# Performance work log

Measured on AMD Instinct MI355X. Metric: run time of the kernel, lower is better.

## Reference

```python
import jax, jax.numpy as jnp
import numpy as np

NUM_GRAPHS = 256
N_NODES = 128          # nodes per graph (equal-size graphs)
DEG = 16               # average degree
NUM_EDGES = NUM_GRAPHS * N_NODES * DEG
NUM_HEADS = 8
SCALE = 10.0
INF_REPLACE = 1.0


def setup_inputs() -> dict:
    key = jax.random.key(0)
    k1, k2, k3 = jax.random.split(key, 3)
    # each graph owns a contiguous block of N_NODES global node ids
    eg = jnp.repeat(jnp.arange(NUM_GRAPHS, dtype=jnp.int32), N_NODES * DEG)
    src_loc = jax.random.randint(k1, (NUM_EDGES,), 0, N_NODES, dtype=jnp.int32)
    dst_loc = jax.random.randint(k2, (NUM_EDGES,), 0, N_NODES, dtype=jnp.int32)
    edge_index = jnp.stack([eg * N_NODES + src_loc, eg * N_NODES + dst_loc])  # [2, E]
    edge_weight = jax.random.uniform(k3, (NUM_EDGES,), minval=0.1, maxval=1.0)
    batch = jnp.repeat(jnp.arange(NUM_GRAPHS, dtype=jnp.int32), N_NODES)  # [N_total]
    return {
        'edge_index': edge_index,
        'edge_weight': edge_weight,
        'batch': batch,
        'num_graphs': NUM_GRAPHS,
        'max_num_nodes': N_NODES,
    }


def _shortest_path_bias(edge_index, edge_weight, batch, num_graphs, max_num_nodes):
    G, n = num_graphs, max_num_nodes
    inf = jnp.inf
    # per-graph node offsets (graphs occupy contiguous node-id blocks)
    counts = jnp.bincount(batch, length=G)
    offsets = jnp.concatenate([jnp.zeros((1,), counts.dtype), jnp.cumsum(counts)[:-1]])
    src, dst = edge_index[0], edge_index[1]
    eg = batch[src]                              # graph id of each edge
    u = src - offsets[eg]                        # local node ids
    v = dst - offsets[eg]
    # self-loops are skipped in the original (masked to +inf -> no-op under min)
    w = jnp.where(src == dst, inf, edge_weight)

    # init dense distance: inf off-diagonal, 0 on diagonal, edge weights scattered
    dist = jnp.full((G, n, n), inf, dtype=edge_weight.dtype)
    diag = jnp.arange(n)
    dist = dist.at[:, diag, diag].set(0.0)
    dist = dist.at[eg, u, v].min(w)

    # batched Floyd-Warshall: d[i,j] = min(d[i,j], d[i,k] + d[k,j]) for all graphs
    def body(d, k):
        col = jax.lax.dynamic_slice_in_dim(d, k, 1, axis=2)  # [G, n, 1] = d[:, :, k]
        row = jax.lax.dynamic_slice_in_dim(d, k, 1, axis=1)  # [G, 1, n] = d[:, k, :]
        return jnp.minimum(d, col + row), None
    dist, _ = jax.lax.scan(body, dist, jnp.arange(n))

    # replace unreachable with 2 * max finite distance (per graph)
    finite = jnp.isfinite(dist)
    fmax = jnp.max(jnp.where(finite, dist, -inf), axis=(1, 2), keepdims=True)
    unreach = jnp.where(jnp.isfinite(fmax), 2.0 * fmax, INF_REPLACE)
    dist = jnp.where(finite, dist, unreach)

    # normalize per graph and scale
    max_val = jnp.maximum(jnp.max(dist, axis=(1, 2), keepdims=True), 1e-8)
    bias = -SCALE * (dist / max_val)
    bias = jnp.nan_to_num(bias, nan=0.0, posinf=-1e6, neginf=-1e6)

    # expand over heads and flatten to [B*H, n, n]
    bias = jnp.broadcast_to(bias[:, None], (G, NUM_HEADS, n, n))
    return bias.reshape(G * NUM_HEADS, n, n)


def reference(edge_index, edge_weight, batch, num_graphs, max_num_nodes):
    return _shortest_path_bias(edge_index, edge_weight, batch, num_graphs, max_num_nodes)
```

## Files before the change

kernel.cpp:

```cpp
#include <hip/hip_runtime.h>

#define NHEADS 8
#define NN     128
#define NCELL  (NN * NN)
#define NT     512
#define SCALE_F 10.0f

typedef float nfloat4 __attribute__((ext_vector_type(4)));

#define RP_O 0
#define RP_N 2048
#define CP_O 4096
#define CP_N 6144
#define DP   8192
#define DPT  8448
#define RED  8704

template<int CBN>
__device__ __forceinline__ void prep_next(float (&dd)[4][8], float* lds,
                                          const int kbn, const int t,
                                          const int rgrp, const int cgrp)
{
    if ((t >> 6) == kbn) {
        const int q = rgrp & 3;
        #pragma unroll
        for (int rr = 0; rr < 4; ++rr) {
            const int iloc = 4 * q + rr;
            const int sw = iloc & 7;
            #pragma unroll
            for (int c = 0; c < 2; ++c) {
                *reinterpret_cast<float4*>(
                    &lds[RP_O + iloc*128 + (((cgrp + 16*c) ^ sw) << 2)]) =
                    make_float4(dd[rr][c*4+0], dd[rr][c*4+1],
                                dd[rr][c*4+2], dd[rr][c*4+3]);
            }
        }
        const int l = t & 63;
        const int p = (cgrp - 4 * (kbn & 3)) & 15;
        if (p < 4) {
            #pragma unroll
            for (int rr = 0; rr < 4; ++rr) {
                *reinterpret_cast<float4*>(&lds[DP + (4*q+rr)*16 + 4*p]) =
                    make_float4(dd[rr][CBN+0], dd[rr][CBN+1],
                                dd[rr][CBN+2], dd[rr][CBN+3]);
            }
        }
        asm volatile("s_waitcnt lgkmcnt(0)" ::: "memory");
        float T[16];
        const int lr = l & 15;
        #pragma unroll
        for (int c4 = 0; c4 < 4; ++c4) {
            float4 v = *reinterpret_cast<const float4*>(&lds[DP + lr*16 + 4*c4]);
            T[c4*4+0]=v.x; T[c4*4+1]=v.y; T[c4*4+2]=v.z; T[c4*4+3]=v.w;
        }
        #pragma unroll
        for (int k = 0; k < 16; ++k) {
            float rk[16];
            #pragma unroll
            for (int j = 0; j < 16; ++j)
                rk[j] = __int_as_float(
                    __builtin_amdgcn_readlane(__float_as_int(T[j]), k));
            const float dik = T[k];
            #pragma unroll
            for (int j = 0; j < 16; ++j)
                T[j] = fminf(T[j], dik + rk[j]);
        }
        if (l < 16) {
            #pragma unroll
            for (int c4 = 0; c4 < 4; ++c4)
                *reinterpret_cast<float4*>(&lds[DP + l*16 + 4*c4]) =
                    make_float4(T[c4*4], T[c4*4+1], T[c4*4+2], T[c4*4+3]);
            #pragma unroll
            for (int j = 0; j < 16; ++j)
                lds[DPT + j*16 + l] = T[j];
        }
    }
    {
        const int q2 = (cgrp - 4 * kbn) & 15;
        if (q2 < 4) {
            #pragma unroll
            for (int e = 0; e < 4; ++e) {
                const int jj = 4 * q2 + e;
                *reinterpret_cast<float4*>(
                    &lds[CP_O + jj*128 + ((rgrp ^ (jj & 7)) << 2)]) =
                    make_float4(dd[0][CBN+e], dd[1][CBN+e],
                                dd[2][CBN+e], dd[3][CBN+e]);
            }
        }
    }
}

__device__ __forceinline__ void phaseB(float* lds, const int t)
{
    if (t < 256) {
        const float INF = __builtin_huge_valf();
        const int ch   = t & 31;
        const int a2   = (t >> 5) & 3;
        const int isC  = t >> 7;
        const int pbase = isC ? CP_O : RP_O;
        const int dbase = isC ? DP   : DPT;
        const int obase = isC ? CP_N : RP_N;
        float acc[4][4];
        #pragma unroll
        for (int rr = 0; rr < 4; ++rr)
            #pragma unroll
            for (int e = 0; e < 4; ++e) acc[rr][e] = INF;
        #pragma unroll
        for (int k = 0; k < 16; ++k) {
            float4 dt = *reinterpret_cast<const float4*>(&lds[dbase + k*16 + 4*a2]);
            float4 r  = *reinterpret_cast<const float4*>(
                &lds[pbase + k*128 + ((ch ^ (k & 7)) << 2)]);
            const float d[4] = {dt.x, dt.y, dt.z, dt.w};
            const float rv[4] = {r.x, r.y, r.z, r.w};
            #pragma unroll
            for (int rr = 0; rr < 4; ++rr)
                #pragma unroll
                for (int e = 0; e < 4; ++e)
                    acc[rr][e] = fminf(acc[rr][e], d[rr] + rv[e]);
        }
        #pragma unroll
        for (int rr = 0; rr < 4; ++rr) {
            const int a = 4*a2 + rr;
            *reinterpret_cast<float4*>(
                &lds[obase + a*128 + ((ch ^ (a & 7)) << 2)]) =
                make_float4(acc[rr][0], acc[rr][1], acc[rr][2], acc[rr][3]);
        }
    }
}

__device__ __forceinline__ void phaseC(float (&dd)[4][8], float* lds,
                                       const int rgrp, const int cgrp)
{
    #pragma unroll
    for (int kp = 0; kp < 8; ++kp) {
        const int k0 = 2*kp, k1 = 2*kp + 1;
        float4 cp0 = *reinterpret_cast<const float4*>(&lds[CP_N + k0*128 + ((rgrp      ^ (k0&7)) << 2)]);
        float4 r0a = *reinterpret_cast<const float4*>(&lds[RP_N + k0*128 + ((cgrp      ^ (k0&7)) << 2)]);
        float4 r0b = *reinterpret_cast<const float4*>(&lds[RP_N + k0*128 + (((cgrp+16) ^ (k0&7)) << 2)]);
        float4 cp1 = *reinterpret_cast<const float4*>(&lds[CP_N + k1*128 + ((rgrp      ^ (k1&7)) << 2)]);
        float4 r1a = *reinterpret_cast<const float4*>(&lds[RP_N + k1*128 + ((cgrp      ^ (k1&7)) << 2)]);
        float4 r1b = *reinterpret_cast<const float4*>(&lds[RP_N + k1*128 + (((cgrp+16) ^ (k1&7)) << 2)]);
        const float c0[4]  = {cp0.x, cp0.y, cp0.z, cp0.w};
        const float c1[4]  = {cp1.x, cp1.y, cp1.z, cp1.w};
        const float ra0[4] = {r0a.x, r0a.y, r0a.z, r0a.w};
        const float rb0[4] = {r0b.x, r0b.y, r0b.z, r0b.w};
        const float ra1[4] = {r1a.x, r1a.y, r1a.z, r1a.w};
        const float rb1[4] = {r1b.x, r1b.y, r1b.z, r1b.w};
        #pragma unroll
        for (int rr = 0; rr < 4; ++rr) {
            #pragma unroll
            for (int e = 0; e < 4; ++e) {
                dd[rr][e]   = fminf(fminf(dd[rr][e],   c0[rr] + ra0[e]), c1[rr] + ra1[e]);
                dd[rr][4+e] = fminf(fminf(dd[rr][4+e], c0[rr] + rb0[e]), c1[rr] + rb1[e]);
            }
        }
    }
}

__global__ __launch_bounds__(NT)
void spb_fw_kernel(const int* __restrict__ edge_index,
                   const float* __restrict__ edge_weight,
                   const int num_edges, const int epg,
                   float* __restrict__ out)
{
    __shared__ float lds[NCELL];
    const float INF = __builtin_huge_valf();
    const int t    = threadIdx.x;
    const int g    = blockIdx.x;
    const int cgrp = t & 15;
    const int rgrp = t >> 4;

    #pragma unroll
    for (int c = 0; c < 8; ++c) {
        const int m   = t + (c << 9);
        const int i   = m >> 5;
        const int scm = m & 31;
        const int c0  = (scm ^ (i & 7)) << 2;
        float4 v;
        v.x = (c0 + 0 == i) ? 0.0f : INF;
        v.y = (c0 + 1 == i) ? 0.0f : INF;
        v.z = (c0 + 2 == i) ? 0.0f : INF;
        v.w = (c0 + 3 == i) ? 0.0f : INF;
        *reinterpret_cast<float4*>(&lds[m << 2]) = v;
    }
    __syncthreads();

    const int ebase = g * epg;
    for (int e = t; e < epg; e += NT) {
        const int idx = ebase + e;
        const int src = edge_index[idx];
        const int dst = edge_index[num_edges + idx];
        const float w = edge_weight[idx];
        const int u = src - g * NN;
        const int v = dst - g * NN;
        if (u != v && (unsigned)u < (unsigned)NN && (unsigned)v < (unsigned)NN) {
            const int a = (u << 7) + (v ^ ((u & 7) << 2));
            atomicMin(reinterpret_cast<int*>(&lds[a]), __float_as_int(w));
        }
    }
    __syncthreads();

    float dd[4][8];
    #pragma unroll
    for (int rr = 0; rr < 4; ++rr) {
        const int i = (rgrp << 2) + rr;
        const int s = i & 7;
        #pragma unroll
        for (int c = 0; c < 2; ++c) {
            float4 v = *reinterpret_cast<const float4*>(
                &lds[(i << 7) + (((cgrp + 16*c) ^ s) << 2)]);
            dd[rr][c*4+0]=v.x; dd[rr][c*4+1]=v.y; dd[rr][c*4+2]=v.z; dd[rr][c*4+3]=v.w;
        }
    }
    __syncthreads();

    prep_next<0>(dd, lds, 0, t, rgrp, cgrp);
    __syncthreads();
    #pragma unroll
    for (int kb = 0; kb < 8; ++kb) {
        phaseB(lds, t);
        __syncthreads();
        phaseC(dd, lds, rgrp, cgrp);
        if (kb < 7) {
            const int kbn = kb + 1;
            if (kbn < 4) prep_next<0>(dd, lds, kbn, t, rgrp, cgrp);
            else         prep_next<4>(dd, lds, kbn, t, rgrp, cgrp);
        }
        __syncthreads();
    }

    float mF = 0.0f, mA = 0.0f;
    #pragma unroll
    for (int rr = 0; rr < 4; ++rr)
        #pragma unroll
        for (int j = 0; j < 8; ++j) {
            const float v = dd[rr][j];
            mA = fmaxf(mA, v);
            mF = fmaxf(mF, v < INF ? v : 0.0f);
        }
    #pragma unroll
    for (int o = 32; o > 0; o >>= 1) {
        mF = fmaxf(mF, __shfl_xor(mF, o));
        mA = fmaxf(mA, __shfl_xor(mA, o));
    }
    if ((t & 63) == 0) {
        lds[RED + ((t >> 6) << 1)]     = mF;
        lds[RED + ((t >> 6) << 1) + 1] = mA;
    }
    __syncthreads();
    mF = lds[RED]; mA = lds[RED + 1];
    #pragma unroll
    for (int wv = 1; wv < 8; ++wv) {
        mF = fmaxf(mF, lds[RED + wv*2]);
        mA = fmaxf(mA, lds[RED + wv*2 + 1]);
    }
    const float twoF  = 2.0f * mF;
    const float maxv  = fmaxf((mA == INF) ? twoF : mF, 1e-8f);
    const float nscal = -SCALE_F / maxv;

    float* const outg = out + (size_t)g * (NHEADS * NCELL);
    #pragma unroll
    for (int rr = 0; rr < 4; ++rr) {
        const int i = (rgrp << 2) + rr;
        #pragma unroll
        for (int c = 0; c < 2; ++c) {
            nfloat4 v;
            v.x = ((dd[rr][c*4+0] == INF) ? twoF : dd[rr][c*4+0]) * nscal;
            v.y = ((dd[rr][c*4+1] == INF) ? twoF : dd[rr][c*4+1]) * nscal;
            v.z = ((dd[rr][c*4+2] == INF) ? twoF : dd[rr][c*4+2]) * nscal;
            v.w = ((dd[rr][c*4+3] == INF) ? twoF : dd[rr][c*4+3]) * nscal;
            const int o = (i << 7) + (cgrp << 2) + (c << 6);
            #pragma unroll
            for (int h = 0; h < NHEADS; ++h) {
                __builtin_nontemporal_store(
                    v, reinterpret_cast<nfloat4*>(&outg[h * NCELL + o]));
            }
        }
    }
}

extern "C" void kernel_launch(void* const* d_in, const int* in_sizes, int n_in,
                              void* d_out, int out_size, void* d_ws, size_t ws_size,
                              hipStream_t stream)
{
    const int*   edge_index  = (const int*)d_in[0];
    const float* edge_w      = (const float*)d_in[1];
    const int E    = in_sizes[1];
    const int Ntot = in_sizes[2];
    const int G    = Ntot / NN;
    const int epg  = E / G;
    float* out = (float*)d_out;
    spb_fw_kernel<<<G, NT, 0, stream>>>(edge_index, edge_w, E, epg, out);
}
```

Before: 74.99 us.

## Restructure blocked Floyd-Warshall to skip column-panel update and double-buffer panels

Each block step now closes the 16x16 diagonal block, then updates only the row panel and feeds the raw column panel straight into the rank-16 min-plus update, dropping the separate column-panel min-plus pass. Column panels are double-buffered in LDS with a padded stride, so the barrier after panel extraction is removed, though a barrier is added between closure and the row-panel update. The XOR swizzles are replaced by padding or plain layouts, and row-panel and column-panel extraction are now done by whichever threads hold that data rather than a single wave. Correctness depends on the column update being algebraically absorbed into the C-phase. The plain row-panel layout may cause more LDS bank conflicts.

```diff
diff --git a/kernel.cpp b/kernel.cpp
--- a/kernel.cpp
+++ b/kernel.cpp
@@ -10,47 +10,64 @@
 
 #define RP_O 0
 #define RP_N 2048
-#define CP_O 4096
-#define CP_N 6144
-#define DP   8192
-#define DPT  8448
-#define RED  8704
+#define CP_As 4096
+#define CP_Bs 6208
+#define DP   8320
+#define RED  8640
 
 template<int CBN>
-__device__ __forceinline__ void prep_next(float (&dd)[4][8], float* lds,
-                                          const int kbn, const int t,
-                                          const int rgrp, const int cgrp)
-{
-    if ((t >> 6) == kbn) {
+__device__ __forceinline__ void extract_panels(const float (&dd)[4][8], float* lds,
+                                               const int kbn, const int t,
+                                               const int rgrp, const int cgrp,
+                                               const int cpbase)
+{
+    if ((rgrp >> 2) == kbn) {
         const int q = rgrp & 3;
         #pragma unroll
         for (int rr = 0; rr < 4; ++rr) {
             const int iloc = 4 * q + rr;
-            const int sw = iloc & 7;
             #pragma unroll
             for (int c = 0; c < 2; ++c) {
                 *reinterpret_cast<float4*>(
-                    &lds[RP_O + iloc*128 + (((cgrp + 16*c) ^ sw) << 2)]) =
+                    &lds[RP_O + iloc * 128 + (cgrp << 2) + (c << 6)]) =
                     make_float4(dd[rr][c*4+0], dd[rr][c*4+1],
                                 dd[rr][c*4+2], dd[rr][c*4+3]);
             }
         }
-        const int l = t & 63;
-        const int p = (cgrp - 4 * (kbn & 3)) & 15;
-        if (p < 4) {
+        const int p = cgrp - 4 * (kbn & 3);
+        if ((unsigned)p < 4u) {
             #pragma unroll
             for (int rr = 0; rr < 4; ++rr) {
-                *reinterpret_cast<float4*>(&lds[DP + (4*q+rr)*16 + 4*p]) =
+                *reinterpret_cast<float4*>(&lds[DP + (4*q+rr) * 20 + (p << 2)]) =
                     make_float4(dd[rr][CBN+0], dd[rr][CBN+1],
                                 dd[rr][CBN+2], dd[rr][CBN+3]);
             }
         }
+    }
+    {
+        const int q2 = cgrp - 4 * (kbn & 3);
+        if ((unsigned)q2 < 4u) {
+            #pragma unroll
+            for (int e = 0; e < 4; ++e) {
+                const int m = 4 * q2 + e;
+                *reinterpret_cast<float4*>(&lds[cpbase + m * 132 + (rgrp << 2)]) =
+                    make_float4(dd[0][CBN+e], dd[1][CBN+e],
+                                dd[2][CBN+e], dd[3][CBN+e]);
+            }
+        }
+    }
+}
+
+__device__ __forceinline__ void closure(float* lds, const int t, const int kb)
+{
+    if ((t >> 6) == kb) {
         asm volatile("s_waitcnt lgkmcnt(0)" ::: "memory");
+        const int l  = t & 63;
+        const int lr = l & 15;
         float T[16];
-        const int lr = l & 15;
         #pragma unroll
         for (int c4 = 0; c4 < 4; ++c4) {
-            float4 v = *reinterpret_cast<const float4*>(&lds[DP + lr*16 + 4*c4]);
+            float4 v = *reinterpret_cast<const float4*>(&lds[DP + lr*20 + (c4<<2)]);
             T[c4*4+0]=v.x; T[c4*4+1]=v.y; T[c4*4+2]=v.z; T[c4*4+3]=v.w;
         }
         #pragma unroll
@@ -68,78 +85,61 @@
         if (l < 16) {
             #pragma unroll
             for (int c4 = 0; c4 < 4; ++c4)
-                *reinterpret_cast<float4*>(&lds[DP + l*16 + 4*c4]) =
+                *reinterpret_cast<float4*>(&lds[DP + l*20 + (c4<<2)]) =
                     make_float4(T[c4*4], T[c4*4+1], T[c4*4+2], T[c4*4+3]);
-            #pragma unroll
-            for (int j = 0; j < 16; ++j)
-                lds[DPT + j*16 + l] = T[j];
-        }
-    }
-    {
-        const int q2 = (cgrp - 4 * kbn) & 15;
-        if (q2 < 4) {
-            #pragma unroll
-            for (int e = 0; e < 4; ++e) {
-                const int jj = 4 * q2 + e;
-                *reinterpret_cast<float4*>(
-                    &lds[CP_O + jj*128 + ((rgrp ^ (jj & 7)) << 2)]) =
-                    make_float4(dd[0][CBN+e], dd[1][CBN+e],
-                                dd[2][CBN+e], dd[3][CBN+e]);
-            }
-        }
-    }
-}
-
-__device__ __forceinline__ void phaseB(float* lds, const int t)
+        }
+    }
+}
+
+__device__ __forceinline__ void bprime(float* lds, const int t)
 {
     if (t < 256) {
         const float INF = __builtin_huge_valf();
-        const int ch   = t & 31;
-        const int a2   = (t >> 5) & 3;
-        const int isC  = t >> 7;
-        const int pbase = isC ? CP_O : RP_O;
-        const int dbase = isC ? DP   : DPT;
-        const int obase = isC ? CP_N : RP_N;
-        float acc[4][4];
-        #pragma unroll
-        for (int rr = 0; rr < 4; ++rr)
-            #pragma unroll
-            for (int e = 0; e < 4; ++e) acc[rr][e] = INF;
-        #pragma unroll
-        for (int k = 0; k < 16; ++k) {
-            float4 dt = *reinterpret_cast<const float4*>(&lds[dbase + k*16 + 4*a2]);
-            float4 r  = *reinterpret_cast<const float4*>(
-                &lds[pbase + k*128 + ((ch ^ (k & 7)) << 2)]);
-            const float d[4] = {dt.x, dt.y, dt.z, dt.w};
-            const float rv[4] = {r.x, r.y, r.z, r.w};
-            #pragma unroll
-            for (int rr = 0; rr < 4; ++rr)
-                #pragma unroll
-                for (int e = 0; e < 4; ++e)
-                    acc[rr][e] = fminf(acc[rr][e], d[rr] + rv[e]);
-        }
-        #pragma unroll
-        for (int rr = 0; rr < 4; ++rr) {
-            const int a = 4*a2 + rr;
-            *reinterpret_cast<float4*>(
-                &lds[obase + a*128 + ((ch ^ (a & 7)) << 2)]) =
-                make_float4(acc[rr][0], acc[rr][1], acc[rr][2], acc[rr][3]);
-        }
-    }
-}
-
-__device__ __forceinline__ void phaseC(float (&dd)[4][8], float* lds,
-                                       const int rgrp, const int cgrp)
-{
-    #pragma unroll
-    for (int kp = 0; kp < 8; ++kp) {
-        const int k0 = 2*kp, k1 = 2*kp + 1;
-        float4 cp0 = *reinterpret_cast<const float4*>(&lds[CP_N + k0*128 + ((rgrp      ^ (k0&7)) << 2)]);
-        float4 r0a = *reinterpret_cast<const float4*>(&lds[RP_N + k0*128 + ((cgrp      ^ (k0&7)) << 2)]);
-        float4 r0b = *reinterpret_cast<const float4*>(&lds[RP_N + k0*128 + (((cgrp+16) ^ (k0&7)) << 2)]);
-        float4 cp1 = *reinterpret_cast<const float4*>(&lds[CP_N + k1*128 + ((rgrp      ^ (k1&7)) << 2)]);
-        float4 r1a = *reinterpret_cast<const float4*>(&lds[RP_N + k1*128 + ((cgrp      ^ (k1&7)) << 2)]);
-        float4 r1b = *reinterpret_cast<const float4*>(&lds[RP_N + k1*128 + (((cgrp+16) ^ (k1&7)) << 2)]);
+        const int k2 = t >> 5;
+        const int ch = t & 31;
+        float da[16], db[16];
+        #pragma unroll
+        for (int c4 = 0; c4 < 4; ++c4) {
+            float4 va = *reinterpret_cast<const float4*>(&lds[DP + (2*k2  )*20 + (c4<<2)]);
+            float4 vb = *reinterpret_cast<const float4*>(&lds[DP + (2*k2+1)*20 + (c4<<2)]);
+            da[c4*4+0]=va.x; da[c4*4+1]=va.y; da[c4*4+2]=va.z; da[c4*4+3]=va.w;
+            db[c4*4+0]=vb.x; db[c4*4+1]=vb.y; db[c4*4+2]=vb.z; db[c4*4+3]=vb.w;
+        }
+        float aA[4] = {INF, INF, INF, INF};
+        float aB[4] = {INF, INF, INF, INF};
+        #pragma unroll
+        for (int mp = 0; mp < 8; ++mp) {
+            const int m0 = 2*mp, m1 = 2*mp + 1;
+            float4 r0 = *reinterpret_cast<const float4*>(&lds[RP_O + m0*128 + (ch<<2)]);
+            float4 r1 = *reinterpret_cast<const float4*>(&lds[RP_O + m1*128 + (ch<<2)]);
+            const float rv0[4] = {r0.x, r0.y, r0.z, r0.w};
+            const float rv1[4] = {r1.x, r1.y, r1.z, r1.w};
+            #pragma unroll
+            for (int e = 0; e < 4; ++e) {
+                aA[e] = fminf(fminf(aA[e], da[m0] + rv0[e]), da[m1] + rv1[e]);
+                aB[e] = fminf(fminf(aB[e], db[m0] + rv0[e]), db[m1] + rv1[e]);
+            }
+        }
+        *reinterpret_cast<float4*>(&lds[RP_N + (2*k2  )*128 + (ch<<2)]) =
+            make_float4(aA[0], aA[1], aA[2], aA[3]);
+        *reinterpret_cast<float4*>(&lds[RP_N + (2*k2+1)*128 + (ch<<2)]) =
+            make_float4(aB[0], aB[1], aB[2], aB[3]);
+    }
+}
+
+__device__ __forceinline__ void cphase(float (&dd)[4][8], float* lds,
+                                       const int rgrp, const int cgrp,
+                                       const int cpbase)
+{
+    #pragma unroll
+    for (int mp = 0; mp < 8; ++mp) {
+        const int m0 = 2*mp, m1 = 2*mp + 1;
+        float4 cp0 = *reinterpret_cast<const float4*>(&lds[cpbase + m0*132 + (rgrp<<2)]);
+        float4 cp1 = *reinterpret_cast<const float4*>(&lds[cpbase + m1*132 + (rgrp<<2)]);
+        float4 r0a = *reinterpret_cast<const float4*>(&lds[RP_N + m0*128 + (cgrp<<2)]);
+        float4 r0b = *reinterpret_cast<const float4*>(&lds[RP_N + m0*128 + (cgrp<<2) + 64]);
+        float4 r1a = *reinterpret_cast<const float4*>(&lds[RP_N + m1*128 + (cgrp<<2)]);
+        float4 r1b = *reinterpret_cast<const float4*>(&lds[RP_N + m1*128 + (cgrp<<2) + 64]);
         const float c0[4]  = {cp0.x, cp0.y, cp0.z, cp0.w};
         const float c1[4]  = {cp1.x, cp1.y, cp1.z, cp1.w};
         const float ra0[4] = {r0a.x, r0a.y, r0a.z, r0a.w};
@@ -214,20 +214,22 @@
     }
     __syncthreads();
 
-    prep_next<0>(dd, lds, 0, t, rgrp, cgrp);
-    __syncthreads();
+    extract_panels<0>(dd, lds, 0, t, rgrp, cgrp, CP_As);
     #pragma unroll
     for (int kb = 0; kb < 8; ++kb) {
-        phaseB(lds, t);
+        closure(lds, t, kb);
         __syncthreads();
-        phaseC(dd, lds, rgrp, cgrp);
+        bprime(lds, t);
+        __syncthreads();
+        cphase(dd, lds, rgrp, cgrp, (kb & 1) ? CP_Bs : CP_As);
         if (kb < 7) {
             const int kbn = kb + 1;
-            if (kbn < 4) prep_next<0>(dd, lds, kbn, t, rgrp, cgrp);
-            else         prep_next<4>(dd, lds, kbn, t, rgrp, cgrp);
-        }
-        __syncthreads();
-    }
+            const int cpb = (kbn & 1) ? CP_Bs : CP_As;
+            if (kbn < 4) extract_panels<0>(dd, lds, kbn, t, rgrp, cgrp, cpb);
+            else         extract_panels<4>(dd, lds, kbn, t, rgrp, cgrp, cpb);
+        }
+    }
+    __syncthreads();
 
     float mF = 0.0f, mA = 0.0f;
     #pragma unroll
```

Measured after the change: 67.41 us. -10.1%, faster.
